# Optimization experiments

Measured on AMD Instinct MI355X. Metric: run time of the kernel, lower is better.

The kernel has to match this reference:

```python
import jax, jax.numpy as jnp
import numpy as np

H = 12  # num_heads
LN_EPS = 1e-5


def setup_inputs() -> dict:
    key = jax.random.key(0)
    ks = jax.random.split(key, 9)
    B, N, C = 16, 785, 768
    hd = C // H
    s = lambda k, shp, fan: jax.random.normal(k, shp, jnp.float32) * (1.0 / np.sqrt(fan))
    return {
        "x": jax.random.normal(ks[0], (B, N, C), jnp.float32),
        "qkv_w": s(ks[1], (C, 3 * C), C),          # Linear(dim, 3*dim), no bias
        "proj_w": s(ks[2], (C, C), C),
        "proj_b": jnp.zeros((C,), jnp.float32),
        "htp_w": s(ks[3], (hd, C), hd),            # ht_proj: Linear(hd, dim)
        "htp_b": jnp.zeros((C,), jnp.float32),
        "ln_g": jnp.ones((hd,), jnp.float32),      # ht_norm LayerNorm(hd)
        "ln_b": jnp.zeros((hd,), jnp.float32),
        "pos": jax.random.normal(ks[4], (1, H, C), jnp.float32) * 0.02,
    }


def reference(x, qkv_w, proj_w, proj_b, htp_w, htp_b, ln_g, ln_b, pos):
    B, N, C = x.shape
    hd = C // H
    scale = hd ** -0.5

    # head-token construction: per-head mean pool over tokens -> (B, H, hd)
    xh = x.reshape(B, N, H, hd).mean(axis=1)
    ht = (xh @ htp_w + htp_b).reshape(B, H, H, hd)        # ht_proj then split per head
    mu = ht.mean(axis=-1, keepdims=True)
    var = ht.var(axis=-1, keepdims=True)
    ht = (ht - mu) * jax.lax.rsqrt(var + LN_EPS) * ln_g + ln_b
    ht = jax.nn.gelu(ht, approximate=False).reshape(B, H, C) + pos  # + head pos embed

    xa = jnp.concatenate([x, ht], axis=1)                 # (B, T, C), T = N + H
    T = N + H

    qkv = (xa @ qkv_w).reshape(B, T, 3, H, hd)
    q, k, v = (jnp.moveaxis(qkv, 2, 0)[i].transpose(0, 2, 1, 3) for i in range(3))  # (B,H,T,hd)
    attn = jax.nn.softmax(jnp.einsum("bhqd,bhkd->bhqk", q, k) * scale, axis=-1)
    out = jnp.einsum("bhqk,bhkd->bhqd", attn, v).transpose(0, 2, 1, 3).reshape(B, T, C)
    out = out @ proj_w + proj_b

    cls = out[:, :1] + out[:, N:].mean(axis=1, keepdims=True)  # cls += mean of head tokens
    return jnp.concatenate([cls, out[:, 1:N]], axis=1)         # (B, N, C)
```

## Files before the change

### kernel.cpp

```cpp
#include <hip/hip_runtime.h>
#include <hip/hip_bf16.h>
#include <math.h>

#define Bsz 16
#define Ntok 785
#define Cdim 768
#define Hn 12
#define HD 64
#define Ttok 797
#define Kdim 768
#define K3C 2304
#define LN_EPS 1e-5f
#define Mrows (Bsz * Ttok)
#define NQS 3
#define NPARTS 5

typedef _Float16 f16;
typedef __attribute__((ext_vector_type(8))) _Float16 half8;
typedef __attribute__((ext_vector_type(4))) _Float16 half4v;
typedef __attribute__((ext_vector_type(8))) unsigned short ushort8;
typedef __attribute__((ext_vector_type(4))) float f32x4;

__device__ inline float wave_sum(float v) {
    #pragma unroll
    for (int off = 32; off; off >>= 1) v += __shfl_xor(v, off, 64);
    return v;
}

#define SW(row) (((((row) & 7) ^ (((row) >> 3) & 7))) << 3)

__global__ void prep_x(const float* __restrict__ x, f16* __restrict__ xa,
                       float* __restrict__ partial) {
    int b = blockIdx.x, ch = blockIdx.y, t = threadIdx.x;
    int n0 = ch * 50, n1 = min(Ntok, n0 + 50);
    float s0 = 0.f, s1 = 0.f, s2 = 0.f;
    for (int n = n0; n < n1; ++n) {
        const float* row = x + ((size_t)b * Ntok + n) * Cdim;
        f16* orow = xa + ((size_t)b * Ttok + n) * Cdim;
        float v0 = row[t], v1 = row[t + 256], v2 = row[t + 512];
        s0 += v0; s1 += v1; s2 += v2;
        orow[t] = (f16)v0; orow[t + 256] = (f16)v1; orow[t + 512] = (f16)v2;
    }
    float* p = partial + ((size_t)b * 16 + ch) * Cdim;
    p[t] = s0; p[t + 256] = s1; p[t + 512] = s2;
}

__global__ void colmean_reduce(const float* __restrict__ partial, float* __restrict__ xh) {
    int b = blockIdx.x, t = threadIdx.x;
    #pragma unroll
    for (int i = 0; i < 3; ++i) {
        int c = t + i * 256;
        float s = 0.f;
        for (int ch = 0; ch < 16; ++ch) s += partial[((size_t)b * 16 + ch) * Cdim + c];
        xh[(size_t)b * Cdim + c] = s * (1.0f / (float)Ntok);
    }
}

__global__ void headtok_kernel(const float* __restrict__ xh, const float* __restrict__ htp_w,
                               const float* __restrict__ htp_b, const float* __restrict__ ln_g,
                               const float* __restrict__ ln_b, const float* __restrict__ pos,
                               f16* __restrict__ xa) {
    int blk = blockIdx.x;
    int b  = blk / (Hn * Hn);
    int rem = blk % (Hn * Hn);
    int h  = rem / Hn;
    int h2 = rem % Hn;
    int lane = threadIdx.x;
    int c = h2 * HD + lane;

    float acc = htp_b[c];
    const float* xrow = xh + (size_t)b * Cdim + h * HD;
    #pragma unroll 8
    for (int d = 0; d < HD; ++d) acc += xrow[d] * htp_w[(size_t)d * Cdim + c];

    float mu = wave_sum(acc) * (1.0f / 64.0f);
    float diff = acc - mu;
    float var = wave_sum(diff * diff) * (1.0f / 64.0f);
    float y = diff * rsqrtf(var + LN_EPS) * ln_g[lane] + ln_b[lane];
    float g = 0.5f * y * (1.0f + erff(y * 0.70710678118654752f));
    float v = g + pos[(size_t)h * Cdim + c];
    xa[((size_t)b * Ttok + Ntok + h) * Cdim + c] = (f16)v;
}

__global__ void convert_wT(const float* __restrict__ W, f16* __restrict__ WT, int K, int N) {
    __shared__ float tile[32][33];
    int nt = blockIdx.x * 32, kt = blockIdx.y * 32;
    int tx = threadIdx.x & 31, ty = threadIdx.x >> 5;
    #pragma unroll
    for (int r = 0; r < 32; r += 8)
        tile[ty + r][tx] = W[(size_t)(kt + ty + r) * N + nt + tx];
    __syncthreads();
    #pragma unroll
    for (int r = 0; r < 32; r += 8) {
        int n = nt + ty + r, k = kt + tx;
        WT[(size_t)n * K + k] = (f16)tile[tx][ty + r];
    }
}

__global__ __launch_bounds__(256, 3)
void mfma_gemm(const f16* __restrict__ A, const f16* __restrict__ W,
               const float* __restrict__ bias, int M, int Nn, int mode, int nNb,
               float* __restrict__ outF, f16* __restrict__ outH) {
    __shared__ __align__(16) f16 smem[3][2][4096];
    const int idx = blockIdx.x;
    const int xcd = idx & 7;
    const int sidx = idx >> 3;
    const int mloc = sidx % 13;
    const int nb = sidx / 13;
    const int cnt = (xcd < 4) ? 13 : 12;
    if (mloc >= cnt) return;
    const int mb = (xcd < 4 ? xcd * 13 : 52 + (xcd - 4) * 12) + mloc;
    const int mBase = mb * 128, nBase = nb * 128;

    const int tid = threadIdx.x;
    const int w = tid >> 6, lane = tid & 63;
    const int lr = lane & 15, lg = lane >> 4;
    const int wr = w >> 1, wc = w & 1;

    const f16* src = (w < 2) ? A : W;
    const int arr = w >> 1;
    const int rowOff = (w & 1) * 64;
    const int rowBase = (w < 2) ? mBase : nBase;
    const int rowMax  = (w < 2) ? (M - 1) : (Nn - 1);
    const int cg = (lane & 3) ^ ((lane >> 2) & 3);
    const int sl8 = (lg ^ (lr & 3)) * 8;

    f32x4 acc[4][4];
    #pragma unroll
    for (int mi = 0; mi < 4; ++mi)
        #pragma unroll
        for (int ni = 0; ni < 4; ++ni) {
            acc[mi][ni][0] = 0.f; acc[mi][ni][1] = 0.f;
            acc[mi][ni][2] = 0.f; acc[mi][ni][3] = 0.f;
        }

    auto stage = [&](int buf, int k0) {
        #pragma unroll
        for (int i = 0; i < 4; ++i) {
            int r16 = rowOff + i * 16;
            int grow = min(rowBase + r16 + (lane >> 2), rowMax);
            const f16* g = src + (size_t)grow * Kdim + k0 + cg * 8;
            f16* l = &smem[buf][arr][r16 * 32];
            __builtin_amdgcn_global_load_lds(
                (const __attribute__((address_space(1))) void*)g,
                (__attribute__((address_space(3))) void*)l, 16, 0, 0);
        }
    };

    const int NT = Kdim / 32;
    stage(0, 0);
    stage(1, 32);
    asm volatile("s_waitcnt vmcnt(4)" ::: "memory");
    __builtin_amdgcn_sched_barrier(0);
    __builtin_amdgcn_s_barrier();
    __builtin_amdgcn_sched_barrier(0);

    int cur = 0;
    for (int t = 0; t < NT; ++t) {
        if (t + 2 < NT) {
            int nbuf = cur + 2; if (nbuf >= 3) nbuf -= 3;
            stage(nbuf, (t + 2) * 32);
        }
        const f16* AS = &smem[cur][0][0];
        const f16* WS = &smem[cur][1][0];
        half8 a[4], b[4];
        #pragma unroll
        for (int mi = 0; mi < 4; ++mi)
            a[mi] = *reinterpret_cast<const half8*>(&AS[(wr * 64 + mi * 16 + lr) * 32 + sl8]);
        #pragma unroll
        for (int ni = 0; ni < 4; ++ni)
            b[ni] = *reinterpret_cast<const half8*>(&WS[(wc * 64 + ni * 16 + lr) * 32 + sl8]);
        #pragma unroll
        for (int mi = 0; mi < 4; ++mi)
            #pragma unroll
            for (int ni = 0; ni < 4; ++ni)
                acc[mi][ni] = __builtin_amdgcn_mfma_f32_16x16x32_f16(a[mi], b[ni], acc[mi][ni], 0, 0, 0);

        if (t + 1 < NT) {
            if (t + 2 < NT)
                asm volatile("s_waitcnt vmcnt(4) lgkmcnt(0)" ::: "memory");
            else
                asm volatile("s_waitcnt vmcnt(0) lgkmcnt(0)" ::: "memory");
            __builtin_amdgcn_sched_barrier(0);
            __builtin_amdgcn_s_barrier();
            __builtin_amdgcn_sched_barrier(0);
        }
        cur = cur + 1; if (cur >= 3) cur -= 3;
    }

    if (mode == 0) {
        #pragma unroll
        for (int ni = 0; ni < 4; ++ni) {
            int gn = nBase + wc * 64 + ni * 16 + lr;
            float bv = bias ? bias[gn] : 0.f;
            #pragma unroll
            for (int mi = 0; mi < 4; ++mi)
                #pragma unroll
                for (int r = 0; r < 4; ++r) {
                    int gm = mBase + wr * 64 + mi * 16 + lg * 4 + r;
                    if (gm < M) outF[(size_t)gm * Nn + gn] = acc[mi][ni][r] + bv;
                }
        }
    } else {
        __syncthreads();
        f16* Ew = &smem[0][0][0] + (size_t)w * 4096;
        #pragma unroll
        for (int mi = 0; mi < 4; ++mi)
            #pragma unroll
            for (int ni = 0; ni < 4; ++ni)
                #pragma unroll
                for (int r = 0; r < 4; ++r) {
                    int er = mi * 16 + lg * 4 + r;
                    int ec = ni * 16 + lr;
                    int chunk = ec >> 3;
                    Ew[er * 64 + ((chunk ^ (er & 7)) << 3) + (ec & 7)] = (f16)acc[mi][ni][r];
                }
        __syncthreads();
        int scol = nBase + wc * 64;
        int s = scol / Cdim;
        int hc = scol - s * Cdim;
        int h = hc >> 6;
        #pragma unroll
        for (int c8 = 0; c8 < 8; ++c8) {
            int er = (lane >> 3) + c8 * 8;
            int chunk = lane & 7;
            half8 v = *reinterpret_cast<const half8*>(&Ew[er * 64 + ((chunk ^ (er & 7)) << 3)]);
            int gm = mBase + wr * 64 + er;
            if (gm < M) {
                int bb = gm / Ttok, tt = gm - bb * Ttok;
                f16* dst = outH + (((size_t)(s * Bsz + bb) * Hn + h) * Ttok + tt) * HD + chunk * 8;
                *reinterpret_cast<half8*>(dst) = v;
            }
        }
    }
}

__global__ __launch_bounds__(256, 2)
void flash_attn_kernel(const f16* __restrict__ Qb, const f16* __restrict__ Kb,
                       const f16* __restrict__ Vb, f16* __restrict__ ao) {
    __shared__ __align__(16) unsigned short KS[64 * 64];
    __shared__ __align__(16) unsigned short VS[64 * 64];

    int bh   = blockIdx.x / NPARTS;
    int part = blockIdx.x % NPARTS;
    int q0 = part * (NQS * 64);
    int smax = min(NQS, (Ttok - q0 + 63) / 64);
    int tid = threadIdx.x;
    int w = tid >> 6, lane = tid & 63;
    int lr = lane & 15, lg = lane >> 4;
    size_t base = (size_t)bh * Ttok * HD;

    half8 qf[NQS][2];
    #pragma unroll
    for (int s = 0; s < NQS; ++s) {
        int qrow = q0 + s * 64 + w * 16 + lr;
        int crow = min(qrow, Ttok - 1);
        #pragma unroll
        for (int kf = 0; kf < 2; ++kf)
            qf[s][kf] = *reinterpret_cast<const half8*>(Qb + base + (size_t)crow * HD + kf * 32 + lg * 8);
    }

    f32x4 O[NQS][4];
    float lsum[NQS];
    #pragma unroll
    for (int s = 0; s < NQS; ++s) {
        lsum[s] = 0.f;
        #pragma unroll
        for (int nt = 0; nt < 4; ++nt) { O[s][nt][0]=0.f; O[s][nt][1]=0.f; O[s][nt][2]=0.f; O[s][nt][3]=0.f; }
    }

    const unsigned short* Kg = (const unsigned short*)(Kb + base);
    const unsigned short* Vg = (const unsigned short*)(Vb + base);

    for (int kt = 0; kt < 13; ++kt) {
        __syncthreads();
        {
            int pr = tid >> 3;
            int g  = tid & 7;
            int k0 = 2 * pr, k1 = k0 + 1;
            int gk0 = kt * 64 + k0;
            ushort8 kv0, kv1, vv0, vv1;
            ushort8 z;
            #pragma unroll
            for (int jj = 0; jj < 8; ++jj) z[jj] = 0;
            if (gk0 < Ttok) {
                kv0 = *reinterpret_cast<const ushort8*>(&Kg[(size_t)gk0 * HD + g * 8]);
                vv0 = *reinterpret_cast<const ushort8*>(&Vg[(size_t)gk0 * HD + g * 8]);
            } else { kv0 = z; vv0 = z; }
            if (gk0 + 1 < Ttok) {
                kv1 = *reinterpret_cast<const ushort8*>(&Kg[(size_t)(gk0 + 1) * HD + g * 8]);
                vv1 = *reinterpret_cast<const ushort8*>(&Vg[(size_t)(gk0 + 1) * HD + g * 8]);
            } else { kv1 = z; vv1 = z; }
            *reinterpret_cast<ushort8*>(&KS[(k0 * 64 + g * 8) ^ SW(k0)]) = kv0;
            *reinterpret_cast<ushort8*>(&KS[(k1 * 64 + g * 8) ^ SW(k1)]) = kv1;
            unsigned* VTd = reinterpret_cast<unsigned*>(VS);
            #pragma unroll
            for (int jj = 0; jj < 8; ++jj) {
                int dim = g * 8 + jj;
                unsigned w2 = (unsigned)vv0[jj] | ((unsigned)vv1[jj] << 16);
                VTd[dim * 32 + (pr ^ ((((dim & 7) ^ ((dim >> 3) & 7))) << 2))] = w2;
            }
        }
        __syncthreads();

        int kbase = kt * 64;
        #pragma unroll
        for (int s = 0; s < NQS; ++s) {
            if (s < smax) {
                half4v pa[4];
                float ls = 0.f;
                #pragma unroll
                for (int ntk = 0; ntk < 4; ++ntk) {
                    f32x4 sc; sc[0]=0.f; sc[1]=0.f; sc[2]=0.f; sc[3]=0.f;
                    #pragma unroll
                    for (int kf = 0; kf < 2; ++kf) {
                        int key = ntk * 16 + lr;
                        int d0 = kf * 32 + lg * 8;
                        half8 k8 = *reinterpret_cast<const half8*>(
                            reinterpret_cast<const f16*>(&KS[(key * 64 + d0) ^ SW(key)]));
                        sc = __builtin_amdgcn_mfma_f32_16x16x32_f16(k8, qf[s][kf], sc, 0, 0, 0);
                    }
                    int kb2 = kbase + ntk * 16 + lg * 4;
                    float p[4];
                    #pragma unroll
                    for (int r = 0; r < 4; ++r) {
                        bool valid = (kb2 + r) < Ttok;
                        p[r] = valid ? __expf(sc[r] * 0.125f - 6.0f) : 0.f;
                        ls += p[r];
                    }
                    auto lo = __builtin_amdgcn_cvt_pkrtz(p[0], p[1]);
                    auto hi = __builtin_amdgcn_cvt_pkrtz(p[2], p[3]);
                    pa[ntk][0] = (f16)lo[0]; pa[ntk][1] = (f16)lo[1];
                    pa[ntk][2] = (f16)hi[0]; pa[ntk][3] = (f16)hi[1];
                }
                lsum[s] += ls;
                #pragma unroll
                for (int ntd = 0; ntd < 4; ++ntd) {
                    int dim = ntd * 16 + lr;
                    #pragma unroll
                    for (int ntk = 0; ntk < 4; ++ntk) {
                        half4v v4 = *reinterpret_cast<const half4v*>(
                            reinterpret_cast<const f16*>(&VS[(dim * 64 + ntk * 16 + lg * 4) ^ SW(dim)]));
                        O[s][ntd] = __builtin_amdgcn_mfma_f32_16x16x16f16(pa[ntk], v4, O[s][ntd], 0, 0, 0);
                    }
                }
            }
        }
    }

    __syncthreads();
    int b = bh / Hn, h = bh % Hn;
    f16* Ew = reinterpret_cast<f16*>(&KS[(size_t)w * 1024]);
    #pragma unroll
    for (int s = 0; s < NQS; ++s) {
        if (s < smax) {
            float l = lsum[s];
            l += __shfl_xor(l, 16, 64);
            l += __shfl_xor(l, 32, 64);
            float inv[4];
            #pragma unroll
            for (int r = 0; r < 4; ++r)
                inv[r] = 1.0f / __shfl(l, lg * 4 + r, 64);
            #pragma unroll
            for (int nt = 0; nt < 4; ++nt)
                #pragma unroll
                for (int r = 0; r < 4; ++r)
                    Ew[(lg * 4 + r) * 64 + nt * 16 + lr] = (f16)(O[s][nt][r] * inv[r]);
            int row = lane >> 2, seg = lane & 3;
            half8 v0 = *reinterpret_cast<const half8*>(&Ew[row * 64 + seg * 16]);
            half8 v1 = *reinterpret_cast<const half8*>(&Ew[row * 64 + seg * 16 + 8]);
            int qrow = q0 + s * 64 + w * 16 + row;
            if (qrow < Ttok) {
                f16* dst = ao + ((size_t)b * Ttok + qrow) * Cdim + h * HD + seg * 16;
                *reinterpret_cast<half8*>(dst) = v0;
                *reinterpret_cast<half8*>(dst + 8) = v1;
            }
        }
    }
}

__global__ void cls_kernel(const float* __restrict__ out_full, float* __restrict__ out) {
    int b = blockIdx.x, t = threadIdx.x;
    #pragma unroll
    for (int i = 0; i < 3; ++i) {
        int c = t + i * 256;
        float s = out_full[((size_t)b * Ttok) * Cdim + c];
        float hs = 0.f;
        #pragma unroll
        for (int h = 0; h < Hn; ++h)
            hs += out_full[((size_t)b * Ttok + Ntok + h) * Cdim + c];
        out[((size_t)b * Ntok) * Cdim + c] = s + hs * (1.0f / (float)Hn);
    }
}

__global__ void final_copy(const float4* __restrict__ out_full, float4* __restrict__ out) {
    const int C4 = Cdim / 4;
    int total = Bsz * (Ntok - 1) * C4;
    for (int i = blockIdx.x * blockDim.x + threadIdx.x; i < total; i += gridDim.x * blockDim.x) {
        int row = i / C4, c4 = i - row * C4;
        int b = row / (Ntok - 1), n = 1 + row - b * (Ntok - 1);
        out[((size_t)b * Ntok + n) * C4 + c4] = out_full[((size_t)b * Ttok + n) * C4 + c4];
    }
}

extern "C" void kernel_launch(void* const* d_in, const int* in_sizes, int n_in,
                              void* d_out, int out_size, void* d_ws, size_t ws_size,
                              hipStream_t stream) {
    const float* x      = (const float*)d_in[0];
    const float* qkv_w  = (const float*)d_in[1];
    const float* proj_w = (const float*)d_in[2];
    const float* proj_b = (const float*)d_in[3];
    const float* htp_w  = (const float*)d_in[4];
    const float* htp_b  = (const float*)d_in[5];
    const float* ln_g   = (const float*)d_in[6];
    const float* ln_b   = (const float*)d_in[7];
    const float* pos    = (const float*)d_in[8];
    float* out = (float*)d_out;

    const size_t MC = (size_t)Mrows * Cdim;
    const size_t WQ = (size_t)K3C * Kdim;
    const size_t WP = (size_t)Cdim * Kdim;

    f16* qkv   = (f16*)d_ws;
    f16* xa    = qkv + 3 * MC;
    f16* wq    = xa + MC;
    f16* wp    = wq + WQ;
    float* partial = (float*)(wp + WP);
    float* xh      = partial + (size_t)Bsz * 16 * Cdim;
    float* out_full = (float*)qkv;

    prep_x<<<dim3(Bsz, 16), 256, 0, stream>>>(x, xa, partial);
    colmean_reduce<<<Bsz, 256, 0, stream>>>(partial, xh);
    headtok_kernel<<<Bsz * Hn * Hn, 64, 0, stream>>>(xh, htp_w, htp_b, ln_g, ln_b, pos, xa);
    convert_wT<<<dim3(K3C / 32, Kdim / 32), 256, 0, stream>>>(qkv_w, wq, Kdim, K3C);
    convert_wT<<<dim3(Cdim / 32, Kdim / 32), 256, 0, stream>>>(proj_w, wp, Kdim, Cdim);

    mfma_gemm<<<8 * 13 * 18, 256, 0, stream>>>(
        xa, wq, nullptr, Mrows, K3C, 1, 18, nullptr, qkv);

    flash_attn_kernel<<<Bsz * Hn * NPARTS, 256, 0, stream>>>(
        qkv, qkv + MC, qkv + 2 * MC, xa);

    mfma_gemm<<<8 * 13 * 6, 256, 0, stream>>>(
        xa, wp, proj_b, Mrows, Cdim, 0, 6, out_full, nullptr);

    cls_kernel<<<Bsz, 256, 0, stream>>>(out_full, out);
    final_copy<<<2048, 256, 0, stream>>>((const float4*)out_full, (float4*)out);
}
```

Measured before the change: 219.3 us.

## Write projection output directly to final layout and fuse small prep kernels

The projection GEMM epilogue now writes token rows 1..N-1 straight into the output tensor and routes the cls and head-token rows into a small side buffer. This removes the separate full-tensor copy kernel and the extra fp32 intermediate. The column-mean reduction is folded into the head-token kernel using wave shuffles, and the two weight conversions are merged into one launch. The flash-attention key loop also drops its bounds checks on all but the last tile. Together these cut several launches and one large memory pass, at the cost of integer division in the GEMM store path.

```diff
diff --git a/kernel.cpp b/kernel.cpp
--- a/kernel.cpp
+++ b/kernel.cpp
@@ -45,18 +45,7 @@
     p[t] = s0; p[t + 256] = s1; p[t + 512] = s2;
 }
 
-__global__ void colmean_reduce(const float* __restrict__ partial, float* __restrict__ xh) {
-    int b = blockIdx.x, t = threadIdx.x;
-    #pragma unroll
-    for (int i = 0; i < 3; ++i) {
-        int c = t + i * 256;
-        float s = 0.f;
-        for (int ch = 0; ch < 16; ++ch) s += partial[((size_t)b * 16 + ch) * Cdim + c];
-        xh[(size_t)b * Cdim + c] = s * (1.0f / (float)Ntok);
-    }
-}
-
-__global__ void headtok_kernel(const float* __restrict__ xh, const float* __restrict__ htp_w,
+__global__ void headtok_kernel(const float* __restrict__ partial, const float* __restrict__ htp_w,
                                const float* __restrict__ htp_b, const float* __restrict__ ln_g,
                                const float* __restrict__ ln_b, const float* __restrict__ pos,
                                f16* __restrict__ xa) {
@@ -68,10 +57,15 @@
     int lane = threadIdx.x;
     int c = h2 * HD + lane;
 
+    float sx = 0.f;
+    #pragma unroll
+    for (int ch = 0; ch < 16; ++ch)
+        sx += partial[((size_t)b * 16 + ch) * Cdim + h * HD + lane];
+    float xv = sx * (1.0f / (float)Ntok);
+
     float acc = htp_b[c];
-    const float* xrow = xh + (size_t)b * Cdim + h * HD;
     #pragma unroll 8
-    for (int d = 0; d < HD; ++d) acc += xrow[d] * htp_w[(size_t)d * Cdim + c];
+    for (int d = 0; d < HD; ++d) acc += __shfl(xv, d, 64) * htp_w[(size_t)d * Cdim + c];
 
     float mu = wave_sum(acc) * (1.0f / 64.0f);
     float diff = acc - mu;
@@ -82,9 +76,14 @@
     xa[((size_t)b * Ttok + Ntok + h) * Cdim + c] = (f16)v;
 }
 
-__global__ void convert_wT(const float* __restrict__ W, f16* __restrict__ WT, int K, int N) {
+__global__ void convert_both(const float* __restrict__ Wq, f16* __restrict__ WTq,
+                             const float* __restrict__ Wp, f16* __restrict__ WTp) {
     __shared__ float tile[32][33];
-    int nt = blockIdx.x * 32, kt = blockIdx.y * 32;
+    int bx = blockIdx.x;
+    const float* W; f16* WT; int N, nt;
+    if (bx < K3C / 32) { W = Wq; WT = WTq; N = K3C; nt = bx * 32; }
+    else               { W = Wp; WT = WTp; N = Cdim; nt = (bx - K3C / 32) * 32; }
+    int kt = blockIdx.y * 32;
     int tx = threadIdx.x & 31, ty = threadIdx.x >> 5;
     #pragma unroll
     for (int r = 0; r < 32; r += 8)
@@ -93,14 +92,15 @@
     #pragma unroll
     for (int r = 0; r < 32; r += 8) {
         int n = nt + ty + r, k = kt + tx;
-        WT[(size_t)n * K + k] = (f16)tile[tx][ty + r];
+        WT[(size_t)n * Kdim + k] = (f16)tile[tx][ty + r];
     }
 }
 
 __global__ __launch_bounds__(256, 3)
 void mfma_gemm(const f16* __restrict__ A, const f16* __restrict__ W,
                const float* __restrict__ bias, int M, int Nn, int mode, int nNb,
-               float* __restrict__ outF, f16* __restrict__ outH) {
+               float* __restrict__ outF, float* __restrict__ sbuf,
+               f16* __restrict__ outH) {
     __shared__ __align__(16) f16 smem[3][2][4096];
     const int idx = blockIdx.x;
     const int xcd = idx & 7;
@@ -198,7 +198,14 @@
                 #pragma unroll
                 for (int r = 0; r < 4; ++r) {
                     int gm = mBase + wr * 64 + mi * 16 + lg * 4 + r;
-                    if (gm < M) outF[(size_t)gm * Nn + gn] = acc[mi][ni][r] + bv;
+                    if (gm < M) {
+                        int bb = gm / Ttok, tt = gm - bb * Ttok;
+                        float v = acc[mi][ni][r] + bv;
+                        if (tt >= 1 && tt < Ntok)
+                            outF[((size_t)bb * Ntok + tt) * Nn + gn] = v;
+                        else
+                            sbuf[((size_t)bb * 13 + (tt == 0 ? 0 : tt - Ntok + 1)) * Nn + gn] = v;
+                    }
                 }
         }
     } else {
@@ -272,25 +279,35 @@
     const unsigned short* Kg = (const unsigned short*)(Kb + base);
     const unsigned short* Vg = (const unsigned short*)(Vb + base);
 
+    int pr = tid >> 3;
+    int g  = tid & 7;
+
     for (int kt = 0; kt < 13; ++kt) {
+        bool tail = (kt == 12);
         __syncthreads();
         {
-            int pr = tid >> 3;
-            int g  = tid & 7;
             int k0 = 2 * pr, k1 = k0 + 1;
             int gk0 = kt * 64 + k0;
             ushort8 kv0, kv1, vv0, vv1;
-            ushort8 z;
-            #pragma unroll
-            for (int jj = 0; jj < 8; ++jj) z[jj] = 0;
-            if (gk0 < Ttok) {
+            if (!tail) {
                 kv0 = *reinterpret_cast<const ushort8*>(&Kg[(size_t)gk0 * HD + g * 8]);
                 vv0 = *reinterpret_cast<const ushort8*>(&Vg[(size_t)gk0 * HD + g * 8]);
-            } else { kv0 = z; vv0 = z; }
-            if (gk0 + 1 < Ttok) {
                 kv1 = *reinterpret_cast<const ushort8*>(&Kg[(size_t)(gk0 + 1) * HD + g * 8]);
                 vv1 = *reinterpret_cast<const ushort8*>(&Vg[(size_t)(gk0 + 1) * HD + g * 8]);
-            } else { kv1 = z; vv1 = z; }
+            } else {
+                ushort8 z;
+                #pragma unroll
+                for (int jj = 0; jj < 8; ++jj) z[jj] = 0;
+                kv0 = z; vv0 = z; kv1 = z; vv1 = z;
+                if (gk0 < Ttok) {
+                    kv0 = *reinterpret_cast<const ushort8*>(&Kg[(size_t)gk0 * HD + g * 8]);
+                    vv0 = *reinterpret_cast<const ushort8*>(&Vg[(size_t)gk0 * HD + g * 8]);
+                }
+                if (gk0 + 1 < Ttok) {
+                    kv1 = *reinterpret_cast<const ushort8*>(&Kg[(size_t)(gk0 + 1) * HD + g * 8]);
+                    vv1 = *reinterpret_cast<const ushort8*>(&Vg[(size_t)(gk0 + 1) * HD + g * 8]);
+                }
+            }
             *reinterpret_cast<ushort8*>(&KS[(k0 * 64 + g * 8) ^ SW(k0)]) = kv0;
             *reinterpret_cast<ushort8*>(&KS[(k1 * 64 + g * 8) ^ SW(k1)]) = kv1;
             unsigned* VTd = reinterpret_cast<unsigned*>(VS);
@@ -320,13 +337,21 @@
                             reinterpret_cast<const f16*>(&KS[(key * 64 + d0) ^ SW(key)]));
                         sc = __builtin_amdgcn_mfma_f32_16x16x32_f16(k8, qf[s][kf], sc, 0, 0, 0);
                     }
-                    int kb2 = kbase + ntk * 16 + lg * 4;
                     float p[4];
-                    #pragma unroll
-                    for (int r = 0; r < 4; ++r) {
-                        bool valid = (kb2 + r) < Ttok;
-                        p[r] = valid ? __expf(sc[r] * 0.125f - 6.0f) : 0.f;
-                        ls += p[r];
+                    if (!tail) {
+                        #pragma unroll
+                        for (int r = 0; r < 4; ++r) {
+                            p[r] = __expf(sc[r] * 0.125f - 6.0f);
+                            ls += p[r];
+                        }
+                    } else {
+                        int kb2 = kbase + ntk * 16 + lg * 4;
+                        #pragma unroll
+                        for (int r = 0; r < 4; ++r) {
+                            bool valid = (kb2 + r) < Ttok;
+                            p[r] = valid ? __expf(sc[r] * 0.125f - 6.0f) : 0.f;
+                            ls += p[r];
+                        }
                     }
                     auto lo = __builtin_amdgcn_cvt_pkrtz(p[0], p[1]);
                     auto hi = __builtin_amdgcn_cvt_pkrtz(p[2], p[3]);
@@ -379,27 +404,17 @@
     }
 }
 
-__global__ void cls_kernel(const float* __restrict__ out_full, float* __restrict__ out) {
+__global__ void cls2_kernel(const float* __restrict__ sbuf, float* __restrict__ out) {
     int b = blockIdx.x, t = threadIdx.x;
     #pragma unroll
     for (int i = 0; i < 3; ++i) {
         int c = t + i * 256;
-        float s = out_full[((size_t)b * Ttok) * Cdim + c];
+        float s = sbuf[((size_t)b * 13) * Cdim + c];
         float hs = 0.f;
         #pragma unroll
         for (int h = 0; h < Hn; ++h)
-            hs += out_full[((size_t)b * Ttok + Ntok + h) * Cdim + c];
+            hs += sbuf[((size_t)b * 13 + 1 + h) * Cdim + c];
         out[((size_t)b * Ntok) * Cdim + c] = s + hs * (1.0f / (float)Hn);
-    }
-}
-
-__global__ void final_copy(const float4* __restrict__ out_full, float4* __restrict__ out) {
-    const int C4 = Cdim / 4;
-    int total = Bsz * (Ntok - 1) * C4;
-    for (int i = blockIdx.x * blockDim.x + threadIdx.x; i < total; i += gridDim.x * blockDim.x) {
-        int row = i / C4, c4 = i - row * C4;
-        int b = row / (Ntok - 1), n = 1 + row - b * (Ntok - 1);
-        out[((size_t)b * Ntok + n) * C4 + c4] = out_full[((size_t)b * Ttok + n) * C4 + c4];
     }
 }
 
@@ -426,24 +441,20 @@
     f16* wq    = xa + MC;
     f16* wp    = wq + WQ;
     float* partial = (float*)(wp + WP);
-    float* xh      = partial + (size_t)Bsz * 16 * Cdim;
-    float* out_full = (float*)qkv;
+    float* sbuf    = partial + (size_t)Bsz * 16 * Cdim;
 
     prep_x<<<dim3(Bsz, 16), 256, 0, stream>>>(x, xa, partial);
-    colmean_reduce<<<Bsz, 256, 0, stream>>>(partial, xh);
-    headtok_kernel<<<Bsz * Hn * Hn, 64, 0, stream>>>(xh, htp_w, htp_b, ln_g, ln_b, pos, xa);
-    convert_wT<<<dim3(K3C / 32, Kdim / 32), 256, 0, stream>>>(qkv_w, wq, Kdim, K3C);
-    convert_wT<<<dim3(Cdim / 32, Kdim / 32), 256, 0, stream>>>(proj_w, wp, Kdim, Cdim);
+    headtok_kernel<<<Bsz * Hn * Hn, 64, 0, stream>>>(partial, htp_w, htp_b, ln_g, ln_b, pos, xa);
+    convert_both<<<dim3(96, Kdim / 32), 256, 0, stream>>>(qkv_w, wq, proj_w, wp);
 
     mfma_gemm<<<8 * 13 * 18, 256, 0, stream>>>(
-        xa, wq, nullptr, Mrows, K3C, 1, 18, nullptr, qkv);
+        xa, wq, nullptr, Mrows, K3C, 1, 18, nullptr, nullptr, qkv);
 
     flash_attn_kernel<<<Bsz * Hn * NPARTS, 256, 0, stream>>>(
         qkv, qkv + MC, qkv + 2 * MC, xa);
 
     mfma_gemm<<<8 * 13 * 6, 256, 0, stream>>>(
-        xa, wp, proj_b, Mrows, Cdim, 0, 6, out_full, nullptr);
-
-    cls_kernel<<<Bsz, 256, 0, stream>>>(out_full, out);
-    final_copy<<<2048, 256, 0, stream>>>((const float4*)out_full, (float4*)out);
-}
+        xa, wp, proj_b, Mrows, Cdim, 0, 6, out, sbuf, nullptr);
+
+    cls2_kernel<<<Bsz, 256, 0, stream>>>(sbuf, out);
+}
```

Result: faster. 197.6 us (-9.9%).
